# Kernel tuning notes

Hardware: AMD Instinct MI355X
Metric: run time of the kernel (lower is better)

## Reference

```python
import jax, jax.numpy as jnp
import numpy as np

N = 150000        # active voxels
C = 64            # channels
G = 64            # n_groups (depthwise)
CI = C // G       # in channels per group = 1
CO = C // G       # out channels per group = 1
K = 27            # 3x3x3 kernel volume
BS = 2            # batch size
SS = (480, 360, 32)  # spatial shape (z, y, x)


def _build_pairs(rng):
    """Build submanifold conv indice pairs (gather/scatter maps) from real voxel geometry."""
    total = SS[0] * SS[1] * SS[2]
    per_b = N // BS
    idx_list = []
    for b in range(BS):
        flat = rng.choice(total, size=per_b, replace=False)
        z = flat // (SS[1] * SS[2])
        rem = flat % (SS[1] * SS[2])
        y = rem // SS[2]
        x = rem % SS[2]
        idx_list.append(np.stack([np.full(per_b, b), z, y, x], 1))
    indices = np.concatenate(idx_list).astype(np.int64)  # [N, 4] (b,z,y,x)
    mult = np.array([total, SS[1] * SS[2], SS[2], 1], dtype=np.int64)
    keys = indices @ mult
    order = np.argsort(keys)
    sk = keys[order]
    offsets = np.array([(dz, dy, dx) for dz in (-1, 0, 1) for dy in (-1, 0, 1) for dx in (-1, 0, 1)], dtype=np.int64)
    pair_in = np.zeros((K, N), np.int64)
    pair_out = np.zeros((K, N), np.int64)
    mask = np.zeros((K, N), np.bool_)
    ar = np.arange(N, dtype=np.int64)
    for k in range(K):
        nb = indices.copy()
        nb[:, 1:] += offsets[k]
        inb = ((nb[:, 1] >= 0) & (nb[:, 1] < SS[0]) &
               (nb[:, 2] >= 0) & (nb[:, 2] < SS[1]) &
               (nb[:, 3] >= 0) & (nb[:, 3] < SS[2]))
        nk = nb @ mult
        pos = np.clip(np.searchsorted(sk, nk), 0, N - 1)
        found = inb & (sk[pos] == nk)
        j = order[pos]
        pair_in[k] = np.where(found, j, 0)
        pair_out[k] = np.where(found, ar, 0)
        mask[k] = found
    return pair_in, pair_out, mask


def setup_inputs() -> dict:
    rng = np.random.default_rng(0)
    pair_in, pair_out, pair_mask = _build_pairs(rng)
    key = jax.random.key(0)
    kf, kw, kb = jax.random.split(key, 3)
    features = jax.random.normal(kf, (N, C), dtype=jnp.float32)
    weight = jax.random.normal(kw, (K, G, CI, CO), dtype=jnp.float32) * 0.1
    bias = jax.random.normal(kb, (G * CO,), dtype=jnp.float32)
    return {"features": features, "weight": weight, "bias": bias,
            "pair_in": jnp.asarray(pair_in), "pair_out": jnp.asarray(pair_out),
            "pair_mask": jnp.asarray(pair_mask)}


def reference(features, weight, bias, pair_in, pair_out, pair_mask):
    # Grouped submanifold sparse conv: gather -> grouped matmul -> scatter-add,
    # scanned over the K kernel offsets to keep peak memory at O(N*C).
    n = features.shape[0]
    f = features.reshape(n, G, CI)
    mask_f = pair_mask.astype(features.dtype)

    def body(out, kd):
        pin, pout, m, w = kd  # pin/pout: [N], m: [N], w: [G, CI, CO]
        g = f[pin] * m[:, None, None]                 # [N, G, CI] masked gather
        contrib = jnp.einsum('ngc,gco->ngo', g, w)    # grouped matmul
        return out.at[pout].add(contrib), None

    out0 = jnp.zeros((n, G, CO), features.dtype)
    out, _ = jax.lax.scan(body, out0, (pair_in, pair_out, mask_f, weight))
    return out.reshape(n, G * CO) + bias
```

## Files before the change

kernel.cpp:

```cpp
#include <hip/hip_runtime.h>


#define KVOL 27
#define VPW  4
#define WPB  4

__global__ __launch_bounds__(256) void spconv_dw_kernel(
    const float* __restrict__ features,
    const float* __restrict__ weight,
    const float* __restrict__ bias,
    const int* __restrict__ pair_in,
    const int* __restrict__ pair_mask,
    float* __restrict__ out,
    int n)
{
    const int t     = threadIdx.x;
    const int w     = t >> 6;
    const int c     = t & 63;
    const int vbase = blockIdx.x * (VPW * WPB) + w * VPW;

    int   m[VPW], pin13[VPW];
    float fc[VPW];
    #pragma unroll
    for (int s = 0; s < VPW; ++s) { m[s] = 0; pin13[s] = -1; fc[s] = 0.0f; }

    #pragma unroll
    for (int s = 0; s < VPW; ++s) {
        const int vox = vbase + s;
        if (vox < n) {
            if (c < KVOL) m[s] = pair_mask[(size_t)c * n + vox];
            pin13[s] = pair_in[(size_t)13 * n + vox];
            fc[s]    = features[(size_t)vox * 64 + c];
        }
    }

    const float b   = bias[c];
    const float w13 = weight[13 * 64 + c];

    #pragma unroll
    for (int s = 0; s < VPW; ++s) {
        const int vox = vbase + s;
        if (vox >= n) break;

        unsigned long long found = __ballot(m[s] != 0);
        float acc = b;

        if (((found >> 13) & 1ull) && pin13[s] == vox) {
            acc = fmaf(fc[s], w13, acc);
            found &= ~(1ull << 13);
        }

        while (found) {
            const int k = __ffsll(found) - 1;
            found &= found - 1;
            const int pin = pair_in[(size_t)k * n + vox];
            acc = fmaf(features[(size_t)pin * 64 + c], weight[k * 64 + c], acc);
        }

        __builtin_nontemporal_store(acc, &out[(size_t)vox * 64 + c]);
    }
}

extern "C" void kernel_launch(void* const* d_in, const int* in_sizes, int n_in,
                              void* d_out, int out_size, void* d_ws, size_t ws_size,
                              hipStream_t stream) {
    const float* features  = (const float*)d_in[0];
    const float* weight    = (const float*)d_in[1];
    const float* bias      = (const float*)d_in[2];
    const int* pair_in     = (const int*)d_in[3];
    const int* pair_mask   = (const int*)d_in[5];
    float* out             = (float*)d_out;

    const int n = in_sizes[0] / 64;
    const int vpb = VPW * WPB;
    const int blocks = (n + vpb - 1) / vpb;

    spconv_dw_kernel<<<blocks, 256, 0, stream>>>(
        features, weight, bias, pair_in, pair_mask, out, n);
}
```

Baseline: 136.6 us.

## Precompute per-voxel neighbor bitmask in separate kernel before depthwise conv

```diff
diff --git a/kernel.cpp b/kernel.cpp
--- a/kernel.cpp
+++ b/kernel.cpp
@@ -5,12 +5,34 @@
 #define VPW  4
 #define WPB  4
 
+__global__ __launch_bounds__(256) void spconv_meta_kernel(
+    const int* __restrict__ pair_in,
+    const int* __restrict__ pair_mask,
+    unsigned int* __restrict__ bits_ws,
+    int n)
+{
+    const int vox = blockIdx.x * 256 + threadIdx.x;
+    if (vox >= n) return;
+
+    unsigned int bits = 0;
+    #pragma unroll
+    for (int k = 0; k < KVOL; ++k) {
+        const int mv = pair_mask[(size_t)k * n + vox];
+        bits |= (mv != 0 ? 1u : 0u) << k;
+    }
+    const int pin13 = pair_in[(size_t)13 * n + vox];
+    if ((bits & (1u << 13)) && pin13 == vox)
+        bits = (bits & ~(1u << 13)) | 0x80000000u;
+
+    bits_ws[vox] = bits;
+}
+
 __global__ __launch_bounds__(256) void spconv_dw_kernel(
     const float* __restrict__ features,
     const float* __restrict__ weight,
     const float* __restrict__ bias,
     const int* __restrict__ pair_in,
-    const int* __restrict__ pair_mask,
+    const unsigned int* __restrict__ bits_ws,
     float* __restrict__ out,
     int n)
 {
@@ -19,17 +41,16 @@
     const int c     = t & 63;
     const int vbase = blockIdx.x * (VPW * WPB) + w * VPW;
 
-    int   m[VPW], pin13[VPW];
+    unsigned int bitsv[VPW];
     float fc[VPW];
     #pragma unroll
-    for (int s = 0; s < VPW; ++s) { m[s] = 0; pin13[s] = -1; fc[s] = 0.0f; }
+    for (int s = 0; s < VPW; ++s) { bitsv[s] = 0; fc[s] = 0.0f; }
 
     #pragma unroll
     for (int s = 0; s < VPW; ++s) {
         const int vox = vbase + s;
         if (vox < n) {
-            if (c < KVOL) m[s] = pair_mask[(size_t)c * n + vox];
-            pin13[s] = pair_in[(size_t)13 * n + vox];
+            bitsv[s] = bits_ws[vox];
             fc[s]    = features[(size_t)vox * 64 + c];
         }
     }
@@ -42,16 +63,15 @@
         const int vox = vbase + s;
         if (vox >= n) break;
 
-        unsigned long long found = __ballot(m[s] != 0);
+        const unsigned int bv = __builtin_amdgcn_readfirstlane(bitsv[s]);
         float acc = b;
 
-        if (((found >> 13) & 1ull) && pin13[s] == vox) {
+        if (bv & 0x80000000u)
             acc = fmaf(fc[s], w13, acc);
-            found &= ~(1ull << 13);
-        }
 
+        unsigned int found = bv & 0x07FFFFFFu;
         while (found) {
-            const int k = __ffsll(found) - 1;
+            const int k = __builtin_ctz(found);
             found &= found - 1;
             const int pin = pair_in[(size_t)k * n + vox];
             acc = fmaf(features[(size_t)pin * 64 + c], weight[k * 64 + c], acc);
@@ -70,11 +90,15 @@
     const int* pair_in     = (const int*)d_in[3];
     const int* pair_mask   = (const int*)d_in[5];
     float* out             = (float*)d_out;
+    unsigned int* bits_ws  = (unsigned int*)d_ws;
 
     const int n = in_sizes[0] / 64;
+
+    const int blocks1 = (n + 255) / 256;
+    spconv_meta_kernel<<<blocks1, 256, 0, stream>>>(pair_in, pair_mask, bits_ws, n);
+
     const int vpb = VPW * WPB;
-    const int blocks = (n + vpb - 1) / vpb;
-
-    spconv_dw_kernel<<<blocks, 256, 0, stream>>>(
-        features, weight, bias, pair_in, pair_mask, out, n);
+    const int blocks2 = (n + vpb - 1) / vpb;
+    spconv_dw_kernel<<<blocks2, 256, 0, stream>>>(
+        features, weight, bias, pair_in, bits_ws, out, n);
 }
```

Result: faster. 133.7 us (-2.1%).
